# Kernel tuning notes

Hardware: AMD Instinct MI355X
Metric: run time of the kernel (lower is better)

## Reference

```python
import jax, jax.numpy as jnp
import numpy as np

N, E, D_IN, D_H, D_OUT = 50000, 600000, 128, 128, 1


def setup_inputs() -> dict:
    key = jax.random.key(0)
    ks = jax.random.split(key, 20)
    p = lambda k, sh: jax.random.normal(k, sh, dtype=jnp.float32) * 0.05
    return {
        "x": jax.random.normal(ks[0], (N, D_IN), dtype=jnp.float32),
        "edge_weight": jax.random.uniform(ks[1], (E,), dtype=jnp.float32),
        # input LEConv (lin1: W1/b1, lin2: W2 no bias, lin3: W3/b3)
        "W1_in": p(ks[2], (D_IN, D_H)), "b1_in": jnp.zeros((D_H,), jnp.float32),
        "W2_in": p(ks[3], (D_IN, D_H)),
        "W3_in": p(ks[4], (D_IN, D_H)), "b3_in": jnp.zeros((D_H,), jnp.float32),
        # inner LEConv
        "W1_h": p(ks[5], (D_H, D_H)), "b1_h": jnp.zeros((D_H,), jnp.float32),
        "W2_h": p(ks[6], (D_H, D_H)),
        "W3_h": p(ks[7], (D_H, D_H)), "b3_h": jnp.zeros((D_H,), jnp.float32),
        # output LEConv
        "W1_o": p(ks[8], (D_H, D_OUT)), "b1_o": jnp.zeros((D_OUT,), jnp.float32),
        "W2_o": p(ks[9], (D_H, D_OUT)),
        "W3_o": p(ks[10], (D_H, D_OUT)), "b3_o": jnp.zeros((D_OUT,), jnp.float32),
        # LayerNorms
        "g1": jnp.ones((D_H,), jnp.float32), "beta1": jnp.zeros((D_H,), jnp.float32),
        "g2": jnp.ones((D_H,), jnp.float32), "beta2": jnp.zeros((D_H,), jnp.float32),
        "edge_index": jax.random.randint(ks[11], (2, E), 0, N, dtype=jnp.int32),
        "number_of_layers": 4,
    }


def _leconv(x, src, dst, w, W1, b1, W2, W3, b3):
    # PyG LEConv: out_i = lin3(x_i) + sum_{j->i} w_e * (lin1(x_j) - lin2(x_i))
    a = x @ W1 + b1                                   # [N, D_out]
    b = x @ W2                                        # [N, D_out]
    wsum = jax.ops.segment_sum(w, dst, num_segments=N)             # [N]
    agg = jax.ops.segment_sum(w[:, None] * a[src], dst, num_segments=N)  # [N, D_out]
    return agg - b * wsum[:, None] + x @ W3 + b3


def _ln(x, g, b, eps=1e-5):
    m = x.mean(-1, keepdims=True)
    v = x.var(-1, keepdims=True)
    return (x - m) * jax.lax.rsqrt(v + eps) * g + b


def reference(x, edge_weight, W1_in, b1_in, W2_in, W3_in, b3_in,
              W1_h, b1_h, W2_h, W3_h, b3_h,
              W1_o, b1_o, W2_o, W3_o, b3_o,
              g1, beta1, g2, beta2, edge_index, number_of_layers):
    src, dst = edge_index[0], edge_index[1]
    # per-feature standardization over nodes (torch std is unbiased -> ddof=1)
    x = (x - x.mean(0, keepdims=True)) / (jnp.std(x, axis=0, ddof=1, keepdims=True) + 1e-6)
    h = jax.nn.leaky_relu(
        _ln(_leconv(x, src, dst, edge_weight, W1_in, b1_in, W2_in, W3_in, b3_in), g1, beta1),
        negative_slope=0.1)
    for _ in range(number_of_layers - 2):
        h = jax.nn.leaky_relu(
            _ln(_leconv(h, src, dst, edge_weight, W1_h, b1_h, W2_h, W3_h, b3_h), g2, beta2),
            negative_slope=0.1)
    h = _leconv(h, src, dst, edge_weight, W1_o, b1_o, W2_o, W3_o, b3_o)
    return jax.nn.sigmoid(h)
```

## Files before the change

### kernel.cpp

```cpp
#include <hip/hip_runtime.h>
#include <hip/hip_bf16.h>
#include <math.h>


typedef _Float16 f16x8 __attribute__((ext_vector_type(8)));
typedef _Float16 f16x4 __attribute__((ext_vector_type(4)));
typedef float f32x4 __attribute__((ext_vector_type(4)));

#define LSTRIDE 136
#define CS_BLOCKS 512
#define WFIX 8388608.0f


__global__ __launch_bounds__(256) void prep_kernel(
    const float* __restrict__ x, int N,
    float* __restrict__ ps, float* __restrict__ pss,
    const float* __restrict__ W1a, const float* __restrict__ W2a,
    const float* __restrict__ W3a, _Float16* __restrict__ Wta,
    const float* __restrict__ W1b, const float* __restrict__ W2b,
    const float* __restrict__ W3b, _Float16* __restrict__ Wtb,
    unsigned long long* __restrict__ degw, int* __restrict__ counter)
{
    __shared__ float shs[256][4];
    __shared__ float shq[256][4];
    int bid = blockIdx.x;
    int t = threadIdx.x;

    if (bid < CS_BLOCKS) {
        int g = t >> 5;
        int c = t & 31;
        const float4* xv = (const float4*)x;
        const int S = CS_BLOCKS * 8;
        float s0=0.f,s1=0.f,s2=0.f,s3=0.f, q0=0.f,q1=0.f,q2=0.f,q3=0.f;
        int r = bid * 8 + g;
        for (; r + 3*S < N; r += 4*S) {
            float4 v0 = xv[(size_t)r * 32 + c];
            float4 v1 = xv[(size_t)(r + S) * 32 + c];
            float4 v2 = xv[(size_t)(r + 2*S) * 32 + c];
            float4 v3 = xv[(size_t)(r + 3*S) * 32 + c];
            s0 += v0.x + v1.x + v2.x + v3.x;
            s1 += v0.y + v1.y + v2.y + v3.y;
            s2 += v0.z + v1.z + v2.z + v3.z;
            s3 += v0.w + v1.w + v2.w + v3.w;
            q0 += v0.x*v0.x + v1.x*v1.x + v2.x*v2.x + v3.x*v3.x;
            q1 += v0.y*v0.y + v1.y*v1.y + v2.y*v2.y + v3.y*v3.y;
            q2 += v0.z*v0.z + v1.z*v1.z + v2.z*v2.z + v3.z*v3.z;
            q3 += v0.w*v0.w + v1.w*v1.w + v2.w*v2.w + v3.w*v3.w;
        }
        for (; r < N; r += S) {
            float4 v = xv[(size_t)r * 32 + c];
            s0 += v.x; s1 += v.y; s2 += v.z; s3 += v.w;
            q0 += v.x*v.x; q1 += v.y*v.y; q2 += v.z*v.z; q3 += v.w*v.w;
        }
        shs[t][0]=s0; shs[t][1]=s1; shs[t][2]=s2; shs[t][3]=s3;
        shq[t][0]=q0; shq[t][1]=q1; shq[t][2]=q2; shq[t][3]=q3;
        __syncthreads();
        if (t < 32) {
            float S4[4] = {0,0,0,0}, Q4[4] = {0,0,0,0};
            #pragma unroll
            for (int gg = 0; gg < 8; ++gg) {
                #pragma unroll
                for (int i = 0; i < 4; ++i) {
                    S4[i] += shs[t + 32*gg][i];
                    Q4[i] += shq[t + 32*gg][i];
                }
            }
            #pragma unroll
            for (int i = 0; i < 4; ++i) {
                ps [bid * 128 + t*4 + i] = S4[i];
                pss[bid * 128 + t*4 + i] = Q4[i];
            }
        }
        return;
    }

    if (bid < CS_BLOCKS + 384) {
        int idx = (bid - CS_BLOCKS) * 256 + t;
        int set = idx >= 384 * 128;
        int id = idx - set * 384 * 128;
        int n = id >> 7, k = id & 127;
        const float* W = set ? ((n < 128) ? W1b : (n < 256) ? W2b : W3b)
                             : ((n < 128) ? W1a : (n < 256) ? W2a : W3a);
        _Float16* Wt = set ? Wtb : Wta;
        int c = n & 127;
        Wt[id] = (_Float16)W[k * 128 + c];
        return;
    }

    int idx = (bid - CS_BLOCKS - 384) * 256 + t;
    for (int i = idx; i < N; i += 128 * 256) degw[i] = 0ULL;
    if (idx == 0) *counter = 0;
}


__global__ __launch_bounds__(256) void hist_pack_kernel(
    const int* __restrict__ dst, const float* __restrict__ ew,
    unsigned long long* __restrict__ degw, int* __restrict__ rank, int E)
{
    int e = blockIdx.x * 256 + threadIdx.x;
    if (e < E) {
        int d = dst[e];
        unsigned int wf = __float2uint_rn(ew[e] * WFIX);
        unsigned long long old =
            atomicAdd(&degw[d], (1ULL << 32) | (unsigned long long)wf);
        rank[e] = (int)(old >> 32);
    }
}

__global__ __launch_bounds__(256) void scanA_kernel(
    const unsigned long long* __restrict__ degw, int N,
    float* __restrict__ wsum,
    int* __restrict__ partial, int* __restrict__ counter)
{
    __shared__ int sh[256];
    __shared__ int lastFlag;
    int t = threadIdx.x;
    int base = blockIdx.x * 1024 + t * 4;
    int s = 0;
    #pragma unroll
    for (int i = 0; i < 4; ++i) {
        int idx = base + i;
        if (idx < N) {
            unsigned long long v = degw[idx];
            s += (int)(v >> 32);
            wsum[idx] = (float)(unsigned int)v * (1.0f / WFIX);
        }
    }
    sh[t] = s; __syncthreads();
    for (int off = 128; off > 0; off >>= 1) {
        if (t < off) sh[t] += sh[t + off];
        __syncthreads();
    }
    if (t == 0) {
        atomicExch(&partial[blockIdx.x], sh[0]);
        __threadfence();
        int tk = atomicAdd(counter, 1);
        lastFlag = (tk == (int)gridDim.x - 1) ? 1 : 0;
    }
    __syncthreads();
    if (lastFlag && t < 64) {
        __threadfence();
        int nb = (int)gridDim.x;
        int o = (t < nb) ? atomicAdd(&partial[t], 0) : 0;
        int v = o;
        #pragma unroll
        for (int off = 1; off < 64; off <<= 1) {
            int u = __shfl_up(v, off, 64);
            if (t >= off) v += u;
        }
        if (t < nb) atomicExch(&partial[t], v - o);
    }
}

__global__ __launch_bounds__(256) void scan_pass3(
    const unsigned long long* __restrict__ degw, int N,
    const int* __restrict__ partial,
    int* __restrict__ rowptr, int E)
{
    __shared__ int sh[256];
    int t = threadIdx.x;
    int base = blockIdx.x * 1024 + t * 4;
    int v[4]; int s = 0;
    #pragma unroll
    for (int i = 0; i < 4; ++i) {
        int idx = base + i;
        v[i] = (idx < N) ? (int)(degw[idx] >> 32) : 0;
        s += v[i];
    }
    sh[t] = s; __syncthreads();
    for (int off = 1; off < 256; off <<= 1) {
        int x = sh[t];
        if (t >= off) x += sh[t - off];
        __syncthreads();
        sh[t] = x;
        __syncthreads();
    }
    int off0 = partial[blockIdx.x] + ((t > 0) ? sh[t - 1] : 0);
    #pragma unroll
    for (int i = 0; i < 4; ++i) {
        int idx = base + i;
        if (idx < N) { rowptr[idx] = off0; off0 += v[i]; }
    }
    if (blockIdx.x == 0 && t == 0) rowptr[N] = E;
}

__global__ __launch_bounds__(256) void csr_fill_stats_kernel(
    const int* __restrict__ src, const int* __restrict__ dst,
    const float* __restrict__ ew, const int* __restrict__ rowptr,
    const int* __restrict__ rank, int2* __restrict__ csr, int E, int eBlocks,
    const float* __restrict__ ps, const float* __restrict__ pss, int Nn,
    float* __restrict__ mean, float* __restrict__ rstd)
{
    int bid = blockIdx.x;
    int t = threadIdx.x;
    if (bid < eBlocks) {
        int e = bid * 256 + t;
        if (e >= E) return;
        int d = dst[e];
        int pos = rowptr[d] + rank[e];
        csr[pos] = make_int2(src[e], __float_as_int(ew[e]));
        return;
    }
    __shared__ float sh1[256], sh2[256];
    int f = bid - eBlocks;
    int r0 = t * 2;
    float s1 = ps [(size_t)r0 * 128 + f] + ps [(size_t)(r0 + 1) * 128 + f];
    float s2 = pss[(size_t)r0 * 128 + f] + pss[(size_t)(r0 + 1) * 128 + f];
    sh1[t] = s1; sh2[t] = s2; __syncthreads();
    for (int off = 128; off > 0; off >>= 1) {
        if (t < off) { sh1[t] += sh1[t + off]; sh2[t] += sh2[t + off]; }
        __syncthreads();
    }
    if (t == 0) {
        float sum = sh1[0], sumsq = sh2[0];
        float m = sum / (float)Nn;
        float var = (sumsq - sum * sum / (float)Nn) / (float)(Nn - 1);
        var = fmaxf(var, 0.f);
        mean[f] = m;
        rstd[f] = 1.f / (sqrtf(var) + 1e-6f);
    }
}


__global__ __launch_bounds__(256, 2) void gemm_mfma_kernel(
    const _Float16* __restrict__ h, int N, int nTiles,
    const _Float16* __restrict__ Wt,
    const float* __restrict__ b1,
    const float* __restrict__ b3,
    const float* __restrict__ wsum,
    _Float16* __restrict__ out_a, _Float16* __restrict__ out_d)
{
    __shared__ _Float16 ldsS[64 * LSTRIDE];
    __shared__ _Float16 lds_a[64 * LSTRIDE];
    __shared__ _Float16 lds_d[64 * LSTRIDE];

    int t = threadIdx.x;
    int wave = t >> 6;
    int lane = t & 63;
    int quad = lane >> 4;
    int c16  = lane & 15;

    const f16x8* wv = (const f16x8*)Wt;
    int ntl[6] = {2*wave, 2*wave+1, 8+2*wave, 9+2*wave, 16+2*wave, 17+2*wave};
    f16x8 bfrag[6][4];
    #pragma unroll
    for (int j = 0; j < 6; ++j) {
        int nrow = ntl[j] * 16 + c16;
        #pragma unroll
        for (int s = 0; s < 4; ++s)
            bfrag[j][s] = wv[(size_t)nrow * 16 + s * 4 + quad];
    }
    float bb1[2], bb3[2];
    #pragma unroll
    for (int j = 0; j < 2; ++j) {
        int col = (2*wave + j) * 16 + c16;
        bb1[j] = b1[col];
        bb3[j] = b3[col];
    }

    const f16x8* hv = (const f16x8*)h;
    f16x8* oa = (f16x8*)out_a;
    f16x8* od = (f16x8*)out_d;

    for (int tile = blockIdx.x; tile < nTiles; tile += gridDim.x) {
        int row0 = tile * 64;

        #pragma unroll
        for (int i = 0; i < 4; ++i) {
            int idx = i * 256 + t;
            int row = idx >> 4;
            int chunk = idx & 15;
            int grow = row0 + row;
            if (grow >= N) grow = N - 1;
            *(f16x8*)&ldsS[row * LSTRIDE + chunk * 8] = hv[(size_t)grow * 16 + chunk];
        }
        __syncthreads();

        #pragma unroll
        for (int r = 0; r < 4; ++r) {
            f16x8 afrag[4];
            #pragma unroll
            for (int s = 0; s < 4; ++s)
                afrag[s] = *(const f16x8*)&ldsS[(r*16 + c16) * LSTRIDE + (s*4 + quad) * 8];

            f32x4 acc[6];
            #pragma unroll
            for (int j = 0; j < 6; ++j) acc[j] = (f32x4){0.f, 0.f, 0.f, 0.f};
            #pragma unroll
            for (int s = 0; s < 4; ++s) {
                #pragma unroll
                for (int j = 0; j < 6; ++j)
                    acc[j] = __builtin_amdgcn_mfma_f32_16x16x32_f16(afrag[s], bfrag[j][s], acc[j], 0, 0, 0);
            }

            float wsv[4];
            #pragma unroll
            for (int reg = 0; reg < 4; ++reg) {
                int gr = row0 + r*16 + quad*4 + reg;
                wsv[reg] = wsum[(gr < N) ? gr : (N - 1)];
            }
            #pragma unroll
            for (int j = 0; j < 2; ++j) {
                int col = (2*wave + j) * 16 + c16;
                #pragma unroll
                for (int reg = 0; reg < 4; ++reg) {
                    int lr = r*16 + quad*4 + reg;
                    lds_a[lr * LSTRIDE + col] = (_Float16)(acc[j][reg] + bb1[j]);
                    lds_d[lr * LSTRIDE + col] =
                        (_Float16)(acc[4+j][reg] + bb3[j] - wsv[reg] * acc[2+j][reg]);
                }
            }
        }
        __syncthreads();

        #pragma unroll
        for (int i = 0; i < 4; ++i) {
            int idx = i * 256 + t;
            int row = idx >> 4;
            int c8  = idx & 15;
            int grow = row0 + row;
            if (grow < N) {
                f16x8 va = *(const f16x8*)&lds_a[row * LSTRIDE + c8 * 8];
                oa[(size_t)grow * 16 + c8] = va;
                f16x8 vd = *(const f16x8*)&lds_d[row * LSTRIDE + c8 * 8];
                od[(size_t)grow * 16 + c8] = vd;
            }
        }
        __syncthreads();
    }
}


__global__ __launch_bounds__(256, 2) void gemm_mfma_std_kernel(
    const float* __restrict__ x,
    const float* __restrict__ meanp, const float* __restrict__ rstdp,
    int N, int nTiles,
    const _Float16* __restrict__ Wt,
    const float* __restrict__ b1,
    const float* __restrict__ b3,
    const float* __restrict__ wsum,
    _Float16* __restrict__ out_a, _Float16* __restrict__ out_d)
{
    __shared__ _Float16 ldsS[64 * LSTRIDE];
    __shared__ _Float16 lds_a[64 * LSTRIDE];
    __shared__ _Float16 lds_d[64 * LSTRIDE];

    int t = threadIdx.x;
    int wave = t >> 6;
    int lane = t & 63;
    int quad = lane >> 4;
    int c16  = lane & 15;

    const f16x8* wv = (const f16x8*)Wt;
    int ntl[6] = {2*wave, 2*wave+1, 8+2*wave, 9+2*wave, 16+2*wave, 17+2*wave};
    f16x8 bfrag[6][4];
    #pragma unroll
    for (int j = 0; j < 6; ++j) {
        int nrow = ntl[j] * 16 + c16;
        #pragma unroll
        for (int s = 0; s < 4; ++s)
            bfrag[j][s] = wv[(size_t)nrow * 16 + s * 4 + quad];
    }
    float bb1[2], bb3[2];
    #pragma unroll
    for (int j = 0; j < 2; ++j) {
        int col = (2*wave + j) * 16 + c16;
        bb1[j] = b1[col];
        bb3[j] = b3[col];
    }

    int c4 = t & 31;
    float4 mu = ((const float4*)meanp)[c4];
    float4 rs = ((const float4*)rstdp)[c4];

    const float4* xv = (const float4*)x;
    f16x8* oa = (f16x8*)out_a;
    f16x8* od = (f16x8*)out_d;

    for (int tile = blockIdx.x; tile < nTiles; tile += gridDim.x) {
        int row0 = tile * 64;

        #pragma unroll
        for (int i = 0; i < 8; ++i) {
            int idx = i * 256 + t;
            int row = idx >> 5;
            int grow = row0 + row;
            if (grow >= N) grow = N - 1;
            float4 v = xv[(size_t)grow * 32 + c4];
            f16x4 o;
            o.x = (_Float16)((v.x - mu.x) * rs.x);
            o.y = (_Float16)((v.y - mu.y) * rs.y);
            o.z = (_Float16)((v.z - mu.z) * rs.z);
            o.w = (_Float16)((v.w - mu.w) * rs.w);
            *(f16x4*)&ldsS[row * LSTRIDE + c4 * 4] = o;
        }
        __syncthreads();

        #pragma unroll
        for (int r = 0; r < 4; ++r) {
            f16x8 afrag[4];
            #pragma unroll
            for (int s = 0; s < 4; ++s)
                afrag[s] = *(const f16x8*)&ldsS[(r*16 + c16) * LSTRIDE + (s*4 + quad) * 8];

            f32x4 acc[6];
            #pragma unroll
            for (int j = 0; j < 6; ++j) acc[j] = (f32x4){0.f, 0.f, 0.f, 0.f};
            #pragma unroll
            for (int s = 0; s < 4; ++s) {
                #pragma unroll
                for (int j = 0; j < 6; ++j)
                    acc[j] = __builtin_amdgcn_mfma_f32_16x16x32_f16(afrag[s], bfrag[j][s], acc[j], 0, 0, 0);
            }

            float wsv[4];
            #pragma unroll
            for (int reg = 0; reg < 4; ++reg) {
                int gr = row0 + r*16 + quad*4 + reg;
                wsv[reg] = wsum[(gr < N) ? gr : (N - 1)];
            }
            #pragma unroll
            for (int j = 0; j < 2; ++j) {
                int col = (2*wave + j) * 16 + c16;
                #pragma unroll
                for (int reg = 0; reg < 4; ++reg) {
                    int lr = r*16 + quad*4 + reg;
                    lds_a[lr * LSTRIDE + col] = (_Float16)(acc[j][reg] + bb1[j]);
                    lds_d[lr * LSTRIDE + col] =
                        (_Float16)(acc[4+j][reg] + bb3[j] - wsv[reg] * acc[2+j][reg]);
                }
            }
        }
        __syncthreads();

        #pragma unroll
        for (int i = 0; i < 4; ++i) {
            int idx = i * 256 + t;
            int row = idx >> 4;
            int c8  = idx & 15;
            int grow = row0 + row;
            if (grow < N) {
                f16x8 va = *(const f16x8*)&lds_a[row * LSTRIDE + c8 * 8];
                oa[(size_t)grow * 16 + c8] = va;
                f16x8 vd = *(const f16x8*)&lds_d[row * LSTRIDE + c8 * 8];
                od[(size_t)grow * 16 + c8] = vd;
            }
        }
        __syncthreads();
    }
}


__global__ __launch_bounds__(256) void aggregate_ln_kernel(
    const int* __restrict__ rowptr, const int2* __restrict__ csr,
    const _Float16* __restrict__ a, const _Float16* __restrict__ d,
    const float* __restrict__ g, const float* __restrict__ beta,
    _Float16* __restrict__ out, int N)
{
    int wave = threadIdx.x >> 6;
    int lane = threadIdx.x & 63;
    int grp  = lane >> 4;
    int l    = lane & 15;
    int node = blockIdx.x * 4 + wave;
    if (node >= N) return;
    int b = rowptr[node], en = rowptr[node + 1];
    int deg = en - b;

    const f16x8* av = (const f16x8*)a;
    f16x8 dv = ((const f16x8*)d)[(size_t)node * 16 + l];
    float acc[8] = {0,0,0,0,0,0,0,0};

    int nk = (deg + 3) >> 2;
    int k = 0;
    for (; k + 4 <= nk; k += 4) {
        int2 p[4];
        #pragma unroll
        for (int j = 0; j < 4; ++j) {
            int idx = b + (k + j) * 4 + grp;
            int idc = (idx < en) ? idx : b;
            p[j] = csr[idc];
            if (idx >= en) p[j].y = 0;
        }
        f16x8 v[4];
        #pragma unroll
        for (int j = 0; j < 4; ++j)
            v[j] = av[(size_t)p[j].x * 16 + l];
        #pragma unroll
        for (int j = 0; j < 4; ++j) {
            float w = __int_as_float(p[j].y);
            #pragma unroll
            for (int i = 0; i < 8; ++i) acc[i] += w * (float)v[j][i];
        }
    }
    if (k < nk) {
        int2 p[4];
        #pragma unroll
        for (int j = 0; j < 4; ++j) {
            int idx = b + (k + j) * 4 + grp;
            int idc = (idx < en) ? idx : b;
            p[j] = csr[idc];
            if (idx >= en) p[j].y = 0;
        }
        f16x8 v[4];
        #pragma unroll
        for (int j = 0; j < 4; ++j)
            v[j] = av[(size_t)p[j].x * 16 + l];
        #pragma unroll
        for (int j = 0; j < 4; ++j) {
            float w = __int_as_float(p[j].y);
            #pragma unroll
            for (int i = 0; i < 8; ++i) acc[i] += w * (float)v[j][i];
        }
    }

    #pragma unroll
    for (int i = 0; i < 8; ++i) {
        acc[i] += __shfl_xor(acc[i], 16, 64);
        acc[i] += __shfl_xor(acc[i], 32, 64);
    }

    float v[8];
    float s = 0.f, ss = 0.f;
    #pragma unroll
    for (int i = 0; i < 8; ++i) {
        v[i] = acc[i] + (float)dv[i];
        s += v[i]; ss += v[i] * v[i];
    }
    #pragma unroll
    for (int off = 1; off <= 8; off <<= 1) {
        s  += __shfl_xor(s,  off, 64);
        ss += __shfl_xor(ss, off, 64);
    }
    float mean = s * (1.f / 128.f);
    float var = ss * (1.f / 128.f) - mean * mean;
    float rstd = rsqrtf(var + 1e-5f);

    const float4* gv4 = (const float4*)g;
    const float4* bv4 = (const float4*)beta;
    float4 ga = gv4[l*2], gb = gv4[l*2+1];
    float4 ba = bv4[l*2], bb = bv4[l*2+1];
    float go[8] = {ga.x,ga.y,ga.z,ga.w,gb.x,gb.y,gb.z,gb.w};
    float bo[8] = {ba.x,ba.y,ba.z,ba.w,bb.x,bb.y,bb.z,bb.w};
    f16x8 ov;
    #pragma unroll
    for (int i = 0; i < 8; ++i) {
        float o = (v[i] - mean) * rstd * go[i] + bo[i];
        o = o >= 0.f ? o : 0.1f * o;
        ov[i] = (_Float16)o;
    }
    if (grp == 0)
        ((f16x8*)out)[(size_t)node * 16 + l] = ov;
}


__global__ __launch_bounds__(256) void aggregate_out_kernel(
    const int* __restrict__ rowptr, const int2* __restrict__ csr,
    const _Float16* __restrict__ a, const _Float16* __restrict__ d,
    const float* __restrict__ g, const float* __restrict__ beta,
    const float* __restrict__ W1o, const float* __restrict__ b1o,
    const float* __restrict__ W2o,
    const float* __restrict__ W3o, const float* __restrict__ b3o,
    const float* __restrict__ wsum,
    float* __restrict__ a1, float* __restrict__ dpart, int N)
{
    int wave = threadIdx.x >> 6;
    int lane = threadIdx.x & 63;
    int grp  = lane >> 4;
    int l    = lane & 15;
    int node = blockIdx.x * 4 + wave;
    if (node >= N) return;
    int b = rowptr[node], en = rowptr[node + 1];
    int deg = en - b;

    const f16x8* av = (const f16x8*)a;
    f16x8 dv = ((const f16x8*)d)[(size_t)node * 16 + l];
    float wsn = wsum[node];
    float acc[8] = {0,0,0,0,0,0,0,0};

    int nk = (deg + 3) >> 2;
    int k = 0;
    for (; k + 4 <= nk; k += 4) {
        int2 p[4];
        #pragma unroll
        for (int j = 0; j < 4; ++j) {
            int idx = b + (k + j) * 4 + grp;
            int idc = (idx < en) ? idx : b;
            p[j] = csr[idc];
            if (idx >= en) p[j].y = 0;
        }
        f16x8 v[4];
        #pragma unroll
        for (int j = 0; j < 4; ++j)
            v[j] = av[(size_t)p[j].x * 16 + l];
        #pragma unroll
        for (int j = 0; j < 4; ++j) {
            float w = __int_as_float(p[j].y);
            #pragma unroll
            for (int i = 0; i < 8; ++i) acc[i] += w * (float)v[j][i];
        }
    }
    if (k < nk) {
        int2 p[4];
        #pragma unroll
        for (int j = 0; j < 4; ++j) {
            int idx = b + (k + j) * 4 + grp;
            int idc = (idx < en) ? idx : b;
            p[j] = csr[idc];
            if (idx >= en) p[j].y = 0;
        }
        f16x8 v[4];
        #pragma unroll
        for (int j = 0; j < 4; ++j)
            v[j] = av[(size_t)p[j].x * 16 + l];
        #pragma unroll
        for (int j = 0; j < 4; ++j) {
            float w = __int_as_float(p[j].y);
            #pragma unroll
            for (int i = 0; i < 8; ++i) acc[i] += w * (float)v[j][i];
        }
    }

    #pragma unroll
    for (int i = 0; i < 8; ++i) {
        acc[i] += __shfl_xor(acc[i], 16, 64);
        acc[i] += __shfl_xor(acc[i], 32, 64);
    }

    float v[8];
    float s = 0.f, ss = 0.f;
    #pragma unroll
    for (int i = 0; i < 8; ++i) {
        v[i] = acc[i] + (float)dv[i];
        s += v[i]; ss += v[i] * v[i];
    }
    #pragma unroll
    for (int off = 1; off <= 8; off <<= 1) {
        s  += __shfl_xor(s,  off, 64);
        ss += __shfl_xor(ss, off, 64);
    }
    float mean = s * (1.f / 128.f);
    float var = ss * (1.f / 128.f) - mean * mean;
    float rstd = rsqrtf(var + 1e-5f);

    const float4* gv4 = (const float4*)g;
    const float4* bv4 = (const float4*)beta;
    float4 ga = gv4[l*2], gb = gv4[l*2+1];
    float4 ba = bv4[l*2], bb = bv4[l*2+1];
    float go[8] = {ga.x,ga.y,ga.z,ga.w,gb.x,gb.y,gb.z,gb.w};
    float bo[8] = {ba.x,ba.y,ba.z,ba.w,bb.x,bb.y,bb.z,bb.w};

    float ho[8];
    #pragma unroll
    for (int i = 0; i < 8; ++i) {
        float o = (v[i] - mean) * rstd * go[i] + bo[i];
        o = o >= 0.f ? o : 0.1f * o;
        ho[i] = (float)(_Float16)o;
    }

    const float4* w1v = (const float4*)W1o;
    const float4* w2v = (const float4*)W2o;
    const float4* w3v = (const float4*)W3o;
    float4 w1a = w1v[l*2], w1b = w1v[l*2+1];
    float4 w2a = w2v[l*2], w2b = w2v[l*2+1];
    float4 w3a = w3v[l*2], w3b = w3v[l*2+1];
    float s1 = ho[0]*w1a.x + ho[1]*w1a.y + ho[2]*w1a.z + ho[3]*w1a.w
             + ho[4]*w1b.x + ho[5]*w1b.y + ho[6]*w1b.z + ho[7]*w1b.w;
    float s2 = ho[0]*w2a.x + ho[1]*w2a.y + ho[2]*w2a.z + ho[3]*w2a.w
             + ho[4]*w2b.x + ho[5]*w2b.y + ho[6]*w2b.z + ho[7]*w2b.w;
    float s3 = ho[0]*w3a.x + ho[1]*w3a.y + ho[2]*w3a.z + ho[3]*w3a.w
             + ho[4]*w3b.x + ho[5]*w3b.y + ho[6]*w3b.z + ho[7]*w3b.w;
    #pragma unroll
    for (int off = 1; off <= 8; off <<= 1) {
        s1 += __shfl_xor(s1, off, 64);
        s2 += __shfl_xor(s2, off, 64);
        s3 += __shfl_xor(s3, off, 64);
    }
    if (lane == 0) {
        a1[node] = s1 + b1o[0];
        dpart[node] = s3 + b3o[0] - wsn * s2;
    }
}


__global__ __launch_bounds__(256) void gather_out_kernel(
    const int* __restrict__ rowptr, const int2* __restrict__ csr,
    const float* __restrict__ a1, const float* __restrict__ dpart,
    float* __restrict__ out, int N)
{
    int n = blockIdx.x * 256 + threadIdx.x;
    if (n >= N) return;
    int b = rowptr[n], en = rowptr[n + 1];
    float s = dpart[n];
    int e = b;
    for (; e + 4 <= en; e += 4) {
        int2 p0 = csr[e], p1 = csr[e+1], p2 = csr[e+2], p3 = csr[e+3];
        float x0 = a1[p0.x], x1 = a1[p1.x], x2 = a1[p2.x], x3 = a1[p3.x];
        s += __int_as_float(p0.y) * x0 + __int_as_float(p1.y) * x1
           + __int_as_float(p2.y) * x2 + __int_as_float(p3.y) * x3;
    }
    for (; e < en; ++e) {
        int2 p = csr[e];
        s += __int_as_float(p.y) * a1[p.x];
    }
    out[n] = 1.f / (1.f + expf(-s));
}

extern "C" void kernel_launch(void* const* d_in, const int* in_sizes, int n_in,
                              void* d_out, int out_size, void* d_ws, size_t ws_size,
                              hipStream_t stream)
{
    const float* x     = (const float*)d_in[0];
    const float* ew    = (const float*)d_in[1];
    const float* W1_in = (const float*)d_in[2];
    const float* b1_in = (const float*)d_in[3];
    const float* W2_in = (const float*)d_in[4];
    const float* W3_in = (const float*)d_in[5];
    const float* b3_in = (const float*)d_in[6];
    const float* W1_h  = (const float*)d_in[7];
    const float* b1_h  = (const float*)d_in[8];
    const float* W2_h  = (const float*)d_in[9];
    const float* W3_h  = (const float*)d_in[10];
    const float* b3_h  = (const float*)d_in[11];
    const float* W1_o  = (const float*)d_in[12];
    const float* b1_o  = (const float*)d_in[13];
    const float* W2_o  = (const float*)d_in[14];
    const float* W3_o  = (const float*)d_in[15];
    const float* b3_o  = (const float*)d_in[16];
    const float* g1    = (const float*)d_in[17];
    const float* beta1 = (const float*)d_in[18];
    const float* g2    = (const float*)d_in[19];
    const float* beta2 = (const float*)d_in[20];
    const int*   eidx  = (const int*)d_in[21];

    const int N = in_sizes[0] / 128;
    const int E = in_sizes[1];
    const int* srcp = eidx;
    const int* dstp = eidx + E;

    size_t off = 0;
    auto carve = [&](size_t nbytes) -> void* {
        void* p = (char*)d_ws + off;
        off += (nbytes + 255) & ~(size_t)255;
        return p;
    };
    unsigned long long* degw = (unsigned long long*)carve((size_t)N * 8);
    int*      rank   = (int*)     carve((size_t)E * 4);
    _Float16* buf_h  = (_Float16*)carve((size_t)N * 128 * 2);
    _Float16* buf_a  = (_Float16*)carve((size_t)N * 128 * 2);
    _Float16* buf_d  = (_Float16*)carve((size_t)N * 128 * 2);
    int2*     csr    = (int2*)    carve((size_t)E * 8);
    _Float16* Wt_in  = (_Float16*)carve(384 * 128 * 2);
    _Float16* Wt_h   = (_Float16*)carve(384 * 128 * 2);
    int*      rowptr = (int*)     carve((size_t)(N + 1) * 4);
    int*      partial= (int*)     carve(256 * 4);
    int*      counter= (int*)     carve(256 * 4);
    float*    ps     = (float*)   carve((size_t)CS_BLOCKS * 128 * 4);
    float*    pss    = (float*)   carve((size_t)CS_BLOCKS * 128 * 4);
    float*    meanp  = (float*)   carve(128 * 4);
    float*    rstdp  = (float*)   carve(128 * 4);
    float*    wsum   = (float*)   carve((size_t)N * 4);
    float*    a1     = (float*)   carve((size_t)N * 4);
    float*    dpart  = (float*)   carve((size_t)N * 4);

    const int nodeWaveBlocks = (N + 3) / 4;
    const int eBlocks = (E + 255) / 256;
    const int nBlocks = (N + 255) / 256;
    const int nb = (N + 1023) / 1024;

    prep_kernel<<<CS_BLOCKS + 384 + 128, 256, 0, stream>>>(
        x, N, ps, pss,
        W1_in, W2_in, W3_in, Wt_in, W1_h, W2_h, W3_h, Wt_h,
        degw, counter);

    hist_pack_kernel<<<eBlocks, 256, 0, stream>>>(dstp, ew, degw, rank, E);

    scanA_kernel<<<nb, 256, 0, stream>>>(degw, N, wsum, partial, counter);
    scan_pass3<<<nb, 256, 0, stream>>>(degw, N, partial, rowptr, E);

    csr_fill_stats_kernel<<<eBlocks + 128, 256, 0, stream>>>(
        srcp, dstp, ew, rowptr, rank, csr, E, eBlocks,
        ps, pss, N, meanp, rstdp);

    const int nTiles = (N + 63) / 64;
    const int gemmGrid = (nTiles < 512) ? nTiles : 512;

    gemm_mfma_std_kernel<<<gemmGrid, 256, 0, stream>>>(
        x, meanp, rstdp, N, nTiles, Wt_in, b1_in, b3_in, wsum, buf_a, buf_d);
    aggregate_ln_kernel<<<nodeWaveBlocks, 256, 0, stream>>>(rowptr, csr, buf_a, buf_d, g1, beta1, buf_h, N);

    gemm_mfma_kernel<<<gemmGrid, 256, 0, stream>>>(buf_h, N, nTiles, Wt_h, b1_h, b3_h, wsum, buf_a, buf_d);
    aggregate_ln_kernel<<<nodeWaveBlocks, 256, 0, stream>>>(rowptr, csr, buf_a, buf_d, g2, beta2, buf_h, N);

    gemm_mfma_kernel<<<gemmGrid, 256, 0, stream>>>(buf_h, N, nTiles, Wt_h, b1_h, b3_h, wsum, buf_a, buf_d);
    aggregate_out_kernel<<<nodeWaveBlocks, 256, 0, stream>>>(
        rowptr, csr, buf_a, buf_d, g2, beta2,
        W1_o, b1_o, W2_o, W3_o, b3_o, wsum, a1, dpart, N);

    gather_out_kernel<<<nBlocks, 256, 0, stream>>>(rowptr, csr, a1, dpart, (float*)d_out, N);
}
```

Before: 310.9 us.

## Fuse scan passes with grid-wide spin barrier and pad degree counters

Merges the two scan kernels into one. The last block computes the block prefix offsets and raises a flag, and every block spin-waits on that flag before writing rowptr. This removes one kernel launch and a second read of the degree array. Separately, each per-node degree/weight atomic counter is padded to 16 slots (128 bytes) to cut atomic contention on shared cache lines, at the cost of a 16x larger zeroing and a strided read in the scan. The spin barrier assumes all ~49 blocks are co-resident, which holds here but is not guaranteed in general.

```diff
diff --git a/kernel.cpp b/kernel.cpp
--- a/kernel.cpp
+++ b/kernel.cpp
@@ -10,6 +10,7 @@
 #define LSTRIDE 136
 #define CS_BLOCKS 512
 #define WFIX 8388608.0f
+#define DPAD 16
 
 
 __global__ __launch_bounds__(256) void prep_kernel(
@@ -88,8 +89,9 @@
     }
 
     int idx = (bid - CS_BLOCKS - 384) * 256 + t;
-    for (int i = idx; i < N; i += 128 * 256) degw[i] = 0ULL;
-    if (idx == 0) *counter = 0;
+    int tot = N * DPAD;
+    for (int i = idx; i < tot; i += 128 * 256) degw[i] = 0ULL;
+    if (idx == 0) { counter[0] = 0; counter[64] = 0; }
 }
 
 
@@ -102,69 +104,30 @@
         int d = dst[e];
         unsigned int wf = __float2uint_rn(ew[e] * WFIX);
         unsigned long long old =
-            atomicAdd(&degw[d], (1ULL << 32) | (unsigned long long)wf);
+            atomicAdd(&degw[(size_t)d * DPAD], (1ULL << 32) | (unsigned long long)wf);
         rank[e] = (int)(old >> 32);
     }
 }
 
-__global__ __launch_bounds__(256) void scanA_kernel(
+__global__ __launch_bounds__(256) void scan_fused_kernel(
     const unsigned long long* __restrict__ degw, int N,
-    float* __restrict__ wsum,
+    float* __restrict__ wsum, int* __restrict__ rowptr, int E,
     int* __restrict__ partial, int* __restrict__ counter)
 {
     __shared__ int sh[256];
     __shared__ int lastFlag;
+    __shared__ int blockOff;
     int t = threadIdx.x;
     int base = blockIdx.x * 1024 + t * 4;
-    int s = 0;
+    int v[4]; int s = 0;
     #pragma unroll
     for (int i = 0; i < 4; ++i) {
         int idx = base + i;
         if (idx < N) {
-            unsigned long long v = degw[idx];
-            s += (int)(v >> 32);
-            wsum[idx] = (float)(unsigned int)v * (1.0f / WFIX);
-        }
-    }
-    sh[t] = s; __syncthreads();
-    for (int off = 128; off > 0; off >>= 1) {
-        if (t < off) sh[t] += sh[t + off];
-        __syncthreads();
-    }
-    if (t == 0) {
-        atomicExch(&partial[blockIdx.x], sh[0]);
-        __threadfence();
-        int tk = atomicAdd(counter, 1);
-        lastFlag = (tk == (int)gridDim.x - 1) ? 1 : 0;
-    }
-    __syncthreads();
-    if (lastFlag && t < 64) {
-        __threadfence();
-        int nb = (int)gridDim.x;
-        int o = (t < nb) ? atomicAdd(&partial[t], 0) : 0;
-        int v = o;
-        #pragma unroll
-        for (int off = 1; off < 64; off <<= 1) {
-            int u = __shfl_up(v, off, 64);
-            if (t >= off) v += u;
-        }
-        if (t < nb) atomicExch(&partial[t], v - o);
-    }
-}
-
-__global__ __launch_bounds__(256) void scan_pass3(
-    const unsigned long long* __restrict__ degw, int N,
-    const int* __restrict__ partial,
-    int* __restrict__ rowptr, int E)
-{
-    __shared__ int sh[256];
-    int t = threadIdx.x;
-    int base = blockIdx.x * 1024 + t * 4;
-    int v[4]; int s = 0;
-    #pragma unroll
-    for (int i = 0; i < 4; ++i) {
-        int idx = base + i;
-        v[i] = (idx < N) ? (int)(degw[idx] >> 32) : 0;
+            unsigned long long w = degw[(size_t)idx * DPAD];
+            v[i] = (int)(w >> 32);
+            wsum[idx] = (float)(unsigned int)w * (1.0f / WFIX);
+        } else v[i] = 0;
         s += v[i];
     }
     sh[t] = s; __syncthreads();
@@ -175,7 +138,36 @@
         sh[t] = x;
         __syncthreads();
     }
-    int off0 = partial[blockIdx.x] + ((t > 0) ? sh[t - 1] : 0);
+    if (t == 0) {
+        atomicExch(&partial[blockIdx.x], sh[255]);
+        __threadfence();
+        int tk = atomicAdd(&counter[0], 1);
+        lastFlag = (tk == (int)gridDim.x - 1) ? 1 : 0;
+    }
+    __syncthreads();
+    if (lastFlag) {
+        if (t < 64) {
+            __threadfence();
+            int nb = (int)gridDim.x;
+            int o = (t < nb) ? atomicAdd(&partial[t], 0) : 0;
+            int vv = o;
+            #pragma unroll
+            for (int off = 1; off < 64; off <<= 1) {
+                int u = __shfl_up(vv, off, 64);
+                if (t >= off) vv += u;
+            }
+            if (t < nb) atomicExch(&partial[t], vv - o);
+        }
+        __syncthreads();
+        if (t == 0) { __threadfence(); atomicExch(&counter[64], 1); }
+    }
+    if (t == 0) {
+        while (atomicAdd(&counter[64], 0) == 0) {}
+        __threadfence();
+        blockOff = atomicAdd(&partial[blockIdx.x], 0);
+    }
+    __syncthreads();
+    int off0 = blockOff + ((t > 0) ? sh[t - 1] : 0);
     #pragma unroll
     for (int i = 0; i < 4; ++i) {
         int idx = base + i;
@@ -743,7 +735,7 @@
         off += (nbytes + 255) & ~(size_t)255;
         return p;
     };
-    unsigned long long* degw = (unsigned long long*)carve((size_t)N * 8);
+    unsigned long long* degw = (unsigned long long*)carve((size_t)N * DPAD * 8);
     int*      rank   = (int*)     carve((size_t)E * 4);
     _Float16* buf_h  = (_Float16*)carve((size_t)N * 128 * 2);
     _Float16* buf_a  = (_Float16*)carve((size_t)N * 128 * 2);
@@ -774,8 +766,7 @@
 
     hist_pack_kernel<<<eBlocks, 256, 0, stream>>>(dstp, ew, degw, rank, E);
 
-    scanA_kernel<<<nb, 256, 0, stream>>>(degw, N, wsum, partial, counter);
-    scan_pass3<<<nb, 256, 0, stream>>>(degw, N, partial, rowptr, E);
+    scan_fused_kernel<<<nb, 256, 0, stream>>>(degw, N, wsum, rowptr, E, partial, counter);
 
     csr_fill_stats_kernel<<<eBlocks + 128, 256, 0, stream>>>(
         srcp, dstp, ew, rowptr, rank, csr, E, eBlocks,
```

New measurement: 307.1 us. No clear change (-1.2%).
